# Kernel tuning notes

Measured on AMD Instinct MI355X. Metric: run time of the kernel, lower is better.

The kernel has to match this reference:

```python
import jax, jax.numpy as jnp
import numpy as np

TAU = 0.05
MASK_VAL = -1000000000.0
EPS = 1e-12  # torch F.normalize eps


def _l2norm(x):
    n = jnp.linalg.norm(x, axis=-1, keepdims=True)
    return x / jnp.maximum(n, EPS)


def setup_inputs() -> dict:
    key = jax.random.key(0)
    k1, k2 = jax.random.split(key)
    N, D = 16384, 64
    z1 = jax.random.normal(k1, (N, D), dtype=jnp.float32)
    z2 = jax.random.normal(k2, (N, D), dtype=jnp.float32)
    return {"z1": z1, "z2": z2}


def reference(z1, z2):
    # normalize both views
    z1n = _l2norm(z1)
    z2n = _l2norm(z2)
    N = z1n.shape[0]
    # full similarity matrix [N, N]
    sim = jnp.einsum("nd,md->nm", z1n, z2n) / TAU
    pos = jnp.diagonal(sim)  # sim(z1[i], z2[i]) / tau
    # mask the positive position inside the negatives block (as the torch code does)
    eye = jnp.eye(N, dtype=bool)
    neg = jnp.where(eye, MASK_VAL, sim)
    # logits = [pos, masked row]; label = 0 -> CE = logsumexp(logits) - pos
    logits = jnp.concatenate([pos[:, None], neg], axis=1)  # [N, N+1]
    lse = jax.nn.logsumexp(logits, axis=1)
    loss = jnp.sum(lse - pos) / N
    return loss
```

## Files before the change

kernel.cpp:

```cpp
#include <hip/hip_runtime.h>
#include <hip/hip_bf16.h>


typedef __bf16  bf16x8 __attribute__((ext_vector_type(8)));
typedef __bf16  bf16x4 __attribute__((ext_vector_type(4)));
typedef float   f32x4  __attribute__((ext_vector_type(4)));

#if __has_builtin(__builtin_amdgcn_exp2f)
#define EXP2F(x) __builtin_amdgcn_exp2f(x)
#else
#define EXP2F(x) exp2f(x)
#endif
#if __has_builtin(__builtin_amdgcn_logf)
#define LOG2F(x) __builtin_amdgcn_logf(x)
#else
#define LOG2F(x) log2f(x)
#endif

#define DDIM   64
#define TILEB  2048
#define NSETS  4
#define NW     4
#define BM     (NW * NSETS * 16)
#define CS     32

__global__ __launch_bounds__(256) void norm_frag_kernel(
    const float* __restrict__ z1, const float* __restrict__ z2,
    __hip_bfloat16* __restrict__ z1f, __hip_bfloat16* __restrict__ z2f,
    float* __restrict__ rowsum, float* __restrict__ posv,
    float* __restrict__ out, float scale1, int N)
{
    const int tid  = threadIdx.x;
    const int r    = tid >> 4, c = tid & 15;
    const int tile = blockIdx.x;
    const size_t row = (size_t)tile * 16 + r;
    const size_t off = (size_t)tile * TILEB
                     + ((c >> 3) << 10) + (((c >> 1) & 3) << 8)
                     + (r << 4) + ((c & 1) << 3);

    bf16x4 o1, o2;
    {
        float4 v = *(const float4*)(z1 + row * DDIM + c * 4);
        float ss = v.x*v.x + v.y*v.y + v.z*v.z + v.w*v.w;
        #pragma unroll
        for (int o = 8; o; o >>= 1) ss += __shfl_xor(ss, o);
        float inv = scale1 / fmaxf(sqrtf(ss), 1e-12f);
        o1 = (bf16x4){ __float2bfloat16(v.x*inv), __float2bfloat16(v.y*inv),
                       __float2bfloat16(v.z*inv), __float2bfloat16(v.w*inv) };
        *(bf16x4*)((char*)z1f + off) = o1;
    }
    {
        float4 v = *(const float4*)(z2 + row * DDIM + c * 4);
        float ss = v.x*v.x + v.y*v.y + v.z*v.z + v.w*v.w;
        #pragma unroll
        for (int o = 8; o; o >>= 1) ss += __shfl_xor(ss, o);
        float inv = 1.0f / fmaxf(sqrtf(ss), 1e-12f);
        o2 = (bf16x4){ __float2bfloat16(v.x*inv), __float2bfloat16(v.y*inv),
                       __float2bfloat16(v.z*inv), __float2bfloat16(v.w*inv) };
        *(bf16x4*)((char*)z2f + off) = o2;
    }

    float p = (float)o1[0]*(float)o2[0] + (float)o1[1]*(float)o2[1]
            + (float)o1[2]*(float)o2[2] + (float)o1[3]*(float)o2[3];
    #pragma unroll
    for (int o = 8; o; o >>= 1) p += __shfl_xor(p, o);
    if (c == 0) posv[row] = p;

    if (tid < 16) rowsum[(size_t)tile * 16 + tid] = 0.f;
    if (tile == 0 && tid == 0) *out = 0.f;
}

__global__ __launch_bounds__(256, 4) void infonce_main_kernel(
    const __hip_bfloat16* __restrict__ z1f,
    const __hip_bfloat16* __restrict__ z2f,
    float* __restrict__ rowsum,
    int N)
{
    const int tid  = threadIdx.x;
    const int wave = tid >> 6;
    const int lane = tid & 63;
    const int q    = lane >> 4;
    const int l15  = lane & 15;

    const int colspan = N / CS;
    const int ntiles  = colspan >> 4;
    const int c0      = blockIdx.y * colspan;
    const int wr      = blockIdx.x * BM + wave * (NSETS * 16);

    bf16x8 a0[NSETS], a1[NSETS];
    #pragma unroll
    for (int s = 0; s < NSETS; ++s) {
        const char* ab = (const char*)z1f + (size_t)((wr >> 4) + s) * TILEB + lane * 16;
        a0[s] = *(const bf16x8*)(ab);
        a1[s] = *(const bf16x8*)(ab + 1024);
    }

    float sum[NSETS * 4];
    #pragma unroll
    for (int k = 0; k < NSETS * 4; ++k) sum[k] = 0.f;

    const char* bptr = (const char*)z2f + (size_t)(c0 >> 4) * TILEB + lane * 16;
    const f32x4 kzero = {0.f, 0.f, 0.f, 0.f};

    #pragma unroll 4
    for (int t = 0; t < ntiles; ++t) {
        bf16x8 b0 = *(const bf16x8*)(bptr);
        bf16x8 b1 = *(const bf16x8*)(bptr + 1024);
        bptr += TILEB;
        #pragma unroll
        for (int s = 0; s < NSETS; ++s) {
            f32x4 acc = __builtin_amdgcn_mfma_f32_16x16x32_bf16(a0[s], b0, kzero, 0, 0, 0);
            acc = __builtin_amdgcn_mfma_f32_16x16x32_bf16(a1[s], b1, acc, 0, 0, 0);
            sum[s * 4 + 0] += EXP2F(acc[0]);
            sum[s * 4 + 1] += EXP2F(acc[1]);
            sum[s * 4 + 2] += EXP2F(acc[2]);
            sum[s * 4 + 3] += EXP2F(acc[3]);
        }
    }

    #pragma unroll
    for (int k = 0; k < NSETS * 4; ++k) {
        float v = sum[k];
        #pragma unroll
        for (int o = 1; o < 16; o <<= 1) v += __shfl_xor(v, o);
        sum[k] = v;
    }
    if (l15 == 0) {
        #pragma unroll
        for (int s = 0; s < NSETS; ++s)
            #pragma unroll
            for (int i = 0; i < 4; ++i)
                atomicAdd(&rowsum[wr + s * 16 + q * 4 + i], sum[s * 4 + i]);
    }
}

__global__ __launch_bounds__(256) void finalize_kernel(
    const float* __restrict__ rowsum, const float* __restrict__ posv,
    float* __restrict__ out, int N)
{
    int row = blockIdx.x * 256 + threadIdx.x;
    float acc = (LOG2F(rowsum[row]) - posv[row]) * (0.69314718055994531f / (float)N);
    #pragma unroll
    for (int o = 32; o; o >>= 1) acc += __shfl_xor(acc, o);
    if ((threadIdx.x & 63) == 0) atomicAdd(out, acc);
}

extern "C" void kernel_launch(void* const* d_in, const int* in_sizes, int n_in,
                              void* d_out, int out_size, void* d_ws, size_t ws_size,
                              hipStream_t stream)
{
    const float* z1 = (const float*)d_in[0];
    const float* z2 = (const float*)d_in[1];
    const int N = in_sizes[0] / DDIM;

    char* ws = (char*)d_ws;
    __hip_bfloat16* z1f = (__hip_bfloat16*)ws;
    __hip_bfloat16* z2f = z1f + (size_t)N * DDIM;
    float* rowsum = (float*)(ws + 2 * (size_t)N * DDIM * 2);
    float* posv   = rowsum + N;

    const float kScale = 28.853900817779268f;

    norm_frag_kernel<<<N / 16, 256, 0, stream>>>(z1, z2, z1f, z2f, rowsum,
                                                 posv, (float*)d_out, kScale, N);

    dim3 grid(N / BM, CS);
    infonce_main_kernel<<<grid, NW * 64, 0, stream>>>(z1f, z2f, rowsum, N);

    finalize_kernel<<<N / 256, 256, 0, stream>>>(rowsum, posv, (float*)d_out, N);
}
```

Measured before the change: 106.2 us.

## Stage B tiles through double-buffered LDS via direct global-to-LDS loads

Replaces the per-wave global loads of z2 fragment tiles with cooperative global_load_lds transfers into a double-buffered LDS region. Each of the four waves fetches one tile per phase, and all waves then read the four shared tiles from LDS, overlapping the next phase's fetch with the current MFMA and exp work. This cuts redundant global and L2 traffic, since the four waves previously each loaded the same B tiles. The cost is a block-wide barrier and a vmcnt drain every phase, plus 16 KB of LDS that may limit occupancy.

Measured after the change: 108.2 us. No clear change (+1.8%).

```diff
diff --git a/kernel.cpp b/kernel.cpp
--- a/kernel.cpp
+++ b/kernel.cpp
@@ -23,6 +23,13 @@
 #define NW     4
 #define BM     (NW * NSETS * 16)
 #define CS     32
+#define PHT    4
+#define PHB    (PHT * TILEB)
+
+#define GLOAD_LDS(g, l)                                                      \
+    __builtin_amdgcn_global_load_lds(                                        \
+        (const __attribute__((address_space(1))) void*)(g),                  \
+        (__attribute__((address_space(3))) void*)(l), 16, 0, 0)
 
 __global__ __launch_bounds__(256) void norm_frag_kernel(
     const float* __restrict__ z1, const float* __restrict__ z2,
@@ -76,6 +83,8 @@
     float* __restrict__ rowsum,
     int N)
 {
+    __shared__ __align__(16) char ldsb[2 * PHB];
+
     const int tid  = threadIdx.x;
     const int wave = tid >> 6;
     const int lane = tid & 63;
@@ -84,6 +93,7 @@
 
     const int colspan = N / CS;
     const int ntiles  = colspan >> 4;
+    const int nph     = ntiles / PHT;
     const int c0      = blockIdx.y * colspan;
     const int wr      = blockIdx.x * BM + wave * (NSETS * 16);
 
@@ -99,23 +109,44 @@
     #pragma unroll
     for (int k = 0; k < NSETS * 4; ++k) sum[k] = 0.f;
 
-    const char* bptr = (const char*)z2f + (size_t)(c0 >> 4) * TILEB + lane * 16;
+    const char* gB = (const char*)z2f + (size_t)(c0 >> 4) * TILEB;
     const f32x4 kzero = {0.f, 0.f, 0.f, 0.f};
 
-    #pragma unroll 4
-    for (int t = 0; t < ntiles; ++t) {
-        bf16x8 b0 = *(const bf16x8*)(bptr);
-        bf16x8 b1 = *(const bf16x8*)(bptr + 1024);
-        bptr += TILEB;
-        #pragma unroll
-        for (int s = 0; s < NSETS; ++s) {
-            f32x4 acc = __builtin_amdgcn_mfma_f32_16x16x32_bf16(a0[s], b0, kzero, 0, 0, 0);
-            acc = __builtin_amdgcn_mfma_f32_16x16x32_bf16(a1[s], b1, acc, 0, 0, 0);
-            sum[s * 4 + 0] += EXP2F(acc[0]);
-            sum[s * 4 + 1] += EXP2F(acc[1]);
-            sum[s * 4 + 2] += EXP2F(acc[2]);
-            sum[s * 4 + 3] += EXP2F(acc[3]);
+    {
+        const char* src = gB + (size_t)wave * TILEB + (size_t)lane * 16;
+        char*       dst = ldsb + wave * TILEB;
+        GLOAD_LDS(src, dst);
+        GLOAD_LDS(src + 1024, dst + 1024);
+    }
+    asm volatile("s_waitcnt vmcnt(0)" ::: "memory");
+    __syncthreads();
+
+    for (int p = 0; p < nph; ++p) {
+        const int cur = p & 1;
+        if (p + 1 < nph) {
+            const char* src = gB + (size_t)(p + 1) * PHB
+                            + (size_t)wave * TILEB + (size_t)lane * 16;
+            char*       dst = ldsb + (cur ^ 1) * PHB + wave * TILEB;
+            GLOAD_LDS(src, dst);
+            GLOAD_LDS(src + 1024, dst + 1024);
         }
+        const char* bb = ldsb + cur * PHB + lane * 16;
+        #pragma unroll
+        for (int t = 0; t < PHT; ++t) {
+            bf16x8 b0 = *(const bf16x8*)(bb + t * TILEB);
+            bf16x8 b1 = *(const bf16x8*)(bb + t * TILEB + 1024);
+            #pragma unroll
+            for (int s = 0; s < NSETS; ++s) {
+                f32x4 acc = __builtin_amdgcn_mfma_f32_16x16x32_bf16(a0[s], b0, kzero, 0, 0, 0);
+                acc = __builtin_amdgcn_mfma_f32_16x16x32_bf16(a1[s], b1, acc, 0, 0, 0);
+                sum[s * 4 + 0] += EXP2F(acc[0]);
+                sum[s * 4 + 1] += EXP2F(acc[1]);
+                sum[s * 4 + 2] += EXP2F(acc[2]);
+                sum[s * 4 + 3] += EXP2F(acc[3]);
+            }
+        }
+        asm volatile("s_waitcnt vmcnt(0)" ::: "memory");
+        __syncthreads();
     }
 
     #pragma unroll
```
